# Performance work log

Measured on AMD Instinct MI355X. Metric: run time of the kernel, lower is better.

Reference implementation:

```python
import jax, jax.numpy as jnp
import numpy as np

B, S, D = 2, 2048, 1024
N_HEADS = 16
HEAD_DIM = D // N_HEADS


def setup_inputs() -> dict:
    key = jax.random.key(0)
    k1, k2, k3, k4, k5 = jax.random.split(key, 5)
    query = jax.random.normal(k1, (B, S, D), dtype=jnp.float32)
    key_t = jax.random.normal(k2, (B, S, D), dtype=jnp.float32)
    value = jax.random.normal(k3, (B, S, D), dtype=jnp.float32)
    # nn.Linear(dim, 3*dim): weight [3D, D], bias [3D]
    lim = 1.0 / np.sqrt(D)
    W_qkv_w = jax.random.uniform(k4, (3 * D, D), dtype=jnp.float32, minval=-lim, maxval=lim)
    W_qkv_b = jax.random.uniform(k5, (3 * D,), dtype=jnp.float32, minval=-lim, maxval=lim)
    return {"query": query, "key": key_t, "value": value, "W_qkv_w": W_qkv_w, "W_qkv_b": W_qkv_b}


def reference(query, key, value, W_qkv_w, W_qkv_b):
    # key/value args are ignored by the original module: Q, K, V all come
    # from the fused projection of `query` (faithful to source).
    b, s, d = query.shape
    qkv = query @ W_qkv_w.T + W_qkv_b                      # [B, S, 3D]
    qkv = qkv.reshape(b, s, 3, N_HEADS, HEAD_DIM)
    qkv = jnp.transpose(qkv, (2, 0, 3, 1, 4))              # [3, B, H, S, dh]
    q, k, v = qkv[0], qkv[1], qkv[2]
    # Faithful (inverted) scaling: scores DIVIDED by sqrt(1/d_model)
    scale_factor = jnp.sqrt(jnp.asarray(1.0 / (HEAD_DIM * N_HEADS), dtype=query.dtype))
    scores = jnp.einsum('bhqd,bhkd->bhqk', q, k) / scale_factor
    attn = jax.nn.softmax(scores, axis=-1)                 # dropout p=0.0 -> identity
    out = jnp.einsum('bhqk,bhkd->bhqd', attn, v)           # [B, H, S, dh]
    out = jnp.transpose(out, (0, 2, 1, 3)).reshape(b, s, d)
    return out
```

## Files before the change

### kernel.cpp

```cpp
#include <hip/hip_runtime.h>

#define B_  2
#define S_  2048
#define D_  1024
#define H_  16
#define DH_ 64
#define BH_ (B_*H_)

using f32x4   = __attribute__((ext_vector_type(4))) float;
using short4v = __attribute__((ext_vector_type(4))) short;
using short8v = __attribute__((ext_vector_type(8))) short;

__device__ float g_q [(size_t)BH_*S_*DH_];
__device__ float g_k [(size_t)BH_*S_*DH_];
__device__ float g_vt[(size_t)BH_*DH_*S_];

__device__ __forceinline__ short f2bf(float x){
  unsigned u = __builtin_bit_cast(unsigned, x);
  u += 0x7fffu + ((u >> 16) & 1u);
  return (short)(unsigned short)(u >> 16);
}
__device__ __forceinline__ float bf2f(short h){
  return __builtin_bit_cast(float, ((unsigned)(unsigned short)h) << 16);
}
__device__ __forceinline__ void split4f(const float4 v, short4v& h4, short4v& l4){
  float f[4] = {v.x, v.y, v.z, v.w};
#pragma unroll
  for (int i = 0; i < 4; ++i){
    short hh = f2bf(f[i]);
    h4[i] = hh;
    l4[i] = f2bf(f[i] - bf2f(hh));
  }
}

#define MFMA16(A,B,C) __builtin_amdgcn_mfma_f32_16x16x32_bf16((A),(B),(C),0,0,0)

__global__ __launch_bounds__(256) void qkv_proj_mfma(
    const float* __restrict__ X, const float* __restrict__ W,
    const float* __restrict__ bias)
{
  __shared__ short AH[128][40], AL[128][40], BHs[128][40], BLs[128][40];

  const int tid = threadIdx.x;
  const int w  = tid >> 6;
  const int ln = tid & 15;
  const int g  = (tid & 63) >> 4;
  const int wr = w >> 1, wc = w & 1;
  const int m0 = blockIdx.y * 128;
  const int n0 = blockIdx.x * 128;

  f32x4 zero4 = {0.f, 0.f, 0.f, 0.f};
  f32x4 acc[4][4];
#pragma unroll
  for (int mf = 0; mf < 4; ++mf)
#pragma unroll
    for (int nf = 0; nf < 4; ++nf) acc[mf][nf] = zero4;

  for (int k0 = 0; k0 < D_; k0 += 32) {
#pragma unroll
    for (int rep = 0; rep < 4; ++rep) {
      int idx = rep * 256 + tid;
      int r  = idx >> 3;
      int c4 = (idx & 7) << 2;
      float4 a = *(const float4*)&X[(size_t)(m0 + r) * D_ + k0 + c4];
      float4 b = *(const float4*)&W[(size_t)(n0 + r) * D_ + k0 + c4];
      short4v ah4, al4, bh4, bl4;
      split4f(a, ah4, al4);
      split4f(b, bh4, bl4);
      *(short4v*)&AH [r][c4] = ah4;
      *(short4v*)&AL [r][c4] = al4;
      *(short4v*)&BHs[r][c4] = bh4;
      *(short4v*)&BLs[r][c4] = bl4;
    }
    __syncthreads();

    short8v ah[4], al[4], bhf[4], blf[4];
#pragma unroll
    for (int mf = 0; mf < 4; ++mf) {
      ah[mf] = *(const short8v*)&AH[64*wr + 16*mf + ln][8*g];
      al[mf] = *(const short8v*)&AL[64*wr + 16*mf + ln][8*g];
    }
#pragma unroll
    for (int nf = 0; nf < 4; ++nf) {
      bhf[nf] = *(const short8v*)&BHs[64*wc + 16*nf + ln][8*g];
      blf[nf] = *(const short8v*)&BLs[64*wc + 16*nf + ln][8*g];
    }
#pragma unroll
    for (int mf = 0; mf < 4; ++mf)
#pragma unroll
      for (int nf = 0; nf < 4; ++nf) {
        acc[mf][nf] = MFMA16(ah[mf], bhf[nf], acc[mf][nf]);
        acc[mf][nf] = MFMA16(al[mf], bhf[nf], acc[mf][nf]);
        acc[mf][nf] = MFMA16(ah[mf], blf[nf], acc[mf][nf]);
      }
    __syncthreads();
  }

  const int which = n0 >> 10;
#pragma unroll
  for (int nf = 0; nf < 4; ++nf) {
    int col = n0 + 64*wc + 16*nf + ln;
    float bb = bias[col];
    int hh = (col & 1023) >> 6;
    int dh = col & 63;
#pragma unroll
    for (int mf = 0; mf < 4; ++mf) {
      int row0 = m0 + 64*wr + 16*mf + 4*g;
      int bidx = row0 >> 11;
      int s0   = row0 & 2047;
      if (which == 2) {
        f32x4 v;
#pragma unroll
        for (int i = 0; i < 4; ++i) v[i] = acc[mf][nf][i] + bb;
        *(f32x4*)&g_vt[(((size_t)bidx * H_ + hh) * DH_ + dh) * S_ + s0] = v;
      } else {
        float* dst = (which == 0) ? g_q : g_k;
        float sc   = (which == 0) ? 32.0f : 1.0f;
#pragma unroll
        for (int i = 0; i < 4; ++i)
          dst[(((size_t)bidx * H_ + hh) * S_ + s0 + i) * DH_ + dh] =
              (acc[mf][nf][i] + bb) * sc;
      }
    }
  }
}

__global__ __launch_bounds__(256) void attn_mfma(float* __restrict__ out)
{
  __shared__ short KH[64][72], KL[64][72], VT[64][72];
  __shared__ short PS[4][16][72];

  const int tid = threadIdx.x;
  const int w  = tid >> 6;
  const int ln = tid & 15;
  const int g  = (tid & 63) >> 4;
  const int bh = blockIdx.y;
  const int q0 = blockIdx.x * 64;
  const int b  = bh >> 4, h = bh & 15;

  const float* Qp = g_q  + (size_t)bh * S_ * DH_;
  const float* Kp = g_k  + (size_t)bh * S_ * DH_;
  const float* Vp = g_vt + (size_t)bh * DH_ * S_;

  short8v qh[2], ql[2];
  {
    const float* qr = &Qp[(size_t)(q0 + 16*w + ln) * DH_];
#pragma unroll
    for (int ks = 0; ks < 2; ++ks) {
      int d0 = 32*ks + 8*g;
      float4 f0 = *(const float4*)&qr[d0];
      float4 f1 = *(const float4*)&qr[d0 + 4];
      float f[8] = {f0.x,f0.y,f0.z,f0.w,f1.x,f1.y,f1.z,f1.w};
#pragma unroll
      for (int j = 0; j < 8; ++j) {
        short hh = f2bf(f[j]);
        qh[ks][j] = hh;
        ql[ks][j] = f2bf(f[j] - bf2f(hh));
      }
    }
  }

  f32x4 zero4 = {0.f,0.f,0.f,0.f};
  f32x4 o[4];
  float m_[4], l_[4];
#pragma unroll
  for (int i = 0; i < 4; ++i) { o[i] = zero4; m_[i] = -1e30f; l_[i] = 0.f; }

  for (int t0 = 0; t0 < S_; t0 += 64) {
#pragma unroll
    for (int rep = 0; rep < 4; ++rep) {
      int idx = rep * 256 + tid;
      int r  = idx >> 4;
      int c4 = (idx & 15) << 2;
      float4 kv = *(const float4*)&Kp[(size_t)(t0 + r) * DH_ + c4];
      short4v h4, l4;
      split4f(kv, h4, l4);
      *(short4v*)&KH[r][c4] = h4;
      *(short4v*)&KL[r][c4] = l4;
      float4 vv = *(const float4*)&Vp[(size_t)r * S_ + t0 + c4];
      short4v v4;
      v4[0] = f2bf(vv.x); v4[1] = f2bf(vv.y); v4[2] = f2bf(vv.z); v4[3] = f2bf(vv.w);
      *(short4v*)&VT[r][c4] = v4;
    }
    __syncthreads();

    f32x4 s[4];
#pragma unroll
    for (int nf = 0; nf < 4; ++nf) s[nf] = zero4;
#pragma unroll
    for (int ks = 0; ks < 2; ++ks) {
#pragma unroll
      for (int nf = 0; nf < 4; ++nf) {
        const short8v kh = *(const short8v*)&KH[16*nf + ln][32*ks + 8*g];
        const short8v kl = *(const short8v*)&KL[16*nf + ln][32*ks + 8*g];
        s[nf] = MFMA16(qh[ks], kh, s[nf]);
        s[nf] = MFMA16(ql[ks], kh, s[nf]);
        s[nf] = MFMA16(qh[ks], kl, s[nf]);
      }
    }

#pragma unroll
    for (int i = 0; i < 4; ++i) {
      float mt = fmaxf(fmaxf(s[0][i], s[1][i]), fmaxf(s[2][i], s[3][i]));
      mt = fmaxf(mt, __shfl_xor(mt, 1));
      mt = fmaxf(mt, __shfl_xor(mt, 2));
      mt = fmaxf(mt, __shfl_xor(mt, 4));
      mt = fmaxf(mt, __shfl_xor(mt, 8));
      float mn = fmaxf(m_[i], mt);
      float corr = __expf(m_[i] - mn);
      float sum = 0.f;
#pragma unroll
      for (int nf = 0; nf < 4; ++nf) {
        float p = __expf(s[nf][i] - mn);
        sum += p;
        s[nf][i] = p;
      }
      sum += __shfl_xor(sum, 1);
      sum += __shfl_xor(sum, 2);
      sum += __shfl_xor(sum, 4);
      sum += __shfl_xor(sum, 8);
      l_[i] = l_[i] * corr + sum;
      m_[i] = mn;
#pragma unroll
      for (int nf = 0; nf < 4; ++nf) {
        o[nf][i] *= corr;
        PS[w][4*g + i][16*nf + ln] = f2bf(s[nf][i]);
      }
    }

#pragma unroll
    for (int ks = 0; ks < 2; ++ks) {
      const short8v pa = *(const short8v*)&PS[w][ln][32*ks + 8*g];
#pragma unroll
      for (int nf = 0; nf < 4; ++nf) {
        const short8v vb = *(const short8v*)&VT[16*nf + ln][32*ks + 8*g];
        o[nf] = MFMA16(pa, vb, o[nf]);
      }
    }
    __syncthreads();
  }

#pragma unroll
  for (int i = 0; i < 4; ++i) {
    float inv = 1.0f / l_[i];
    int row = q0 + 16*w + 4*g + i;
    float* op = &out[((size_t)b * S_ + row) * D_ + h * DH_];
#pragma unroll
    for (int nf = 0; nf < 4; ++nf)
      op[16*nf + ln] = o[nf][i] * inv;
  }
}

extern "C" void kernel_launch(void* const* d_in, const int* in_sizes, int n_in,
                              void* d_out, int out_size, void* d_ws, size_t ws_size,
                              hipStream_t stream) {
    (void)d_ws; (void)ws_size; (void)n_in; (void)in_sizes;
    const float* X    = (const float*)d_in[0];
    const float* W    = (const float*)d_in[3];
    const float* bias = (const float*)d_in[4];
    float* out = (float*)d_out;

    dim3 gProj(24, 32);
    qkv_proj_mfma<<<gProj, 256, 0, stream>>>(X, W, bias);

    dim3 gAttn(S_ / 64, BH_);
    attn_mfma<<<gAttn, 256, 0, stream>>>(out);
}
```

Before: 306.0 us.

## Store pre-split bf16 Q/K/V, drop LDS staging, enlarge attention query tiles

Result: slower. 347.3 us (+13.5%).

```diff
diff --git a/kernel.cpp b/kernel.cpp
--- a/kernel.cpp
+++ b/kernel.cpp
@@ -6,14 +6,17 @@
 #define H_  16
 #define DH_ 64
 #define BH_ (B_*H_)
+#define NT_ (S_/64)
 
 using f32x4   = __attribute__((ext_vector_type(4))) float;
 using short4v = __attribute__((ext_vector_type(4))) short;
 using short8v = __attribute__((ext_vector_type(8))) short;
 
-__device__ float g_q [(size_t)BH_*S_*DH_];
-__device__ float g_k [(size_t)BH_*S_*DH_];
-__device__ float g_vt[(size_t)BH_*DH_*S_];
+__device__ short g_qh[(size_t)BH_*S_*DH_];
+__device__ short g_ql[(size_t)BH_*S_*DH_];
+__device__ short g_kh[(size_t)BH_*S_*DH_];
+__device__ short g_kl[(size_t)BH_*S_*DH_];
+__device__ short g_vt[(size_t)BH_*DH_*S_];
 
 __device__ __forceinline__ short f2bf(float x){
   unsigned u = __builtin_bit_cast(unsigned, x);
@@ -48,6 +51,7 @@
   const int wr = w >> 1, wc = w & 1;
   const int m0 = blockIdx.y * 128;
   const int n0 = blockIdx.x * 128;
+  const int which = n0 >> 10;
 
   f32x4 zero4 = {0.f, 0.f, 0.f, 0.f};
   f32x4 acc[4][4];
@@ -68,9 +72,11 @@
       split4f(a, ah4, al4);
       split4f(b, bh4, bl4);
       *(short4v*)&AH [r][c4] = ah4;
-      *(short4v*)&AL [r][c4] = al4;
       *(short4v*)&BHs[r][c4] = bh4;
-      *(short4v*)&BLs[r][c4] = bl4;
+      if (which < 2) {
+        *(short4v*)&AL [r][c4] = al4;
+        *(short4v*)&BLs[r][c4] = bl4;
+      }
     }
     __syncthreads();
 
@@ -78,25 +84,26 @@
 #pragma unroll
     for (int mf = 0; mf < 4; ++mf) {
       ah[mf] = *(const short8v*)&AH[64*wr + 16*mf + ln][8*g];
-      al[mf] = *(const short8v*)&AL[64*wr + 16*mf + ln][8*g];
+      if (which < 2) al[mf] = *(const short8v*)&AL[64*wr + 16*mf + ln][8*g];
     }
 #pragma unroll
     for (int nf = 0; nf < 4; ++nf) {
       bhf[nf] = *(const short8v*)&BHs[64*wc + 16*nf + ln][8*g];
-      blf[nf] = *(const short8v*)&BLs[64*wc + 16*nf + ln][8*g];
+      if (which < 2) blf[nf] = *(const short8v*)&BLs[64*wc + 16*nf + ln][8*g];
     }
 #pragma unroll
     for (int mf = 0; mf < 4; ++mf)
 #pragma unroll
       for (int nf = 0; nf < 4; ++nf) {
         acc[mf][nf] = MFMA16(ah[mf], bhf[nf], acc[mf][nf]);
-        acc[mf][nf] = MFMA16(al[mf], bhf[nf], acc[mf][nf]);
-        acc[mf][nf] = MFMA16(ah[mf], blf[nf], acc[mf][nf]);
+        if (which < 2) {
+          acc[mf][nf] = MFMA16(al[mf], bhf[nf], acc[mf][nf]);
+          acc[mf][nf] = MFMA16(ah[mf], blf[nf], acc[mf][nf]);
+        }
       }
     __syncthreads();
   }
 
-  const int which = n0 >> 10;
 #pragma unroll
   for (int nf = 0; nf < 4; ++nf) {
     int col = n0 + 64*wc + 16*nf + ln;
@@ -108,147 +115,171 @@
       int row0 = m0 + 64*wr + 16*mf + 4*g;
       int bidx = row0 >> 11;
       int s0   = row0 & 2047;
+      int bh   = bidx * H_ + hh;
       if (which == 2) {
-        f32x4 v;
-#pragma unroll
-        for (int i = 0; i < 4; ++i) v[i] = acc[mf][nf][i] + bb;
-        *(f32x4*)&g_vt[(((size_t)bidx * H_ + hh) * DH_ + dh) * S_ + s0] = v;
+        short4v v4;
+#pragma unroll
+        for (int i = 0; i < 4; ++i) v4[i] = f2bf(acc[mf][nf][i] + bb);
+        *(short4v*)&g_vt[((size_t)bh * DH_ + dh) * S_ + s0] = v4;
       } else {
-        float* dst = (which == 0) ? g_q : g_k;
-        float sc   = (which == 0) ? 32.0f : 1.0f;
-#pragma unroll
-        for (int i = 0; i < 4; ++i)
-          dst[(((size_t)bidx * H_ + hh) * S_ + s0 + i) * DH_ + dh] =
-              (acc[mf][nf][i] + bb) * sc;
-      }
-    }
-  }
-}
-
-__global__ __launch_bounds__(256) void attn_mfma(float* __restrict__ out)
+        short* dH = (which == 0) ? g_qh : g_kh;
+        short* dL = (which == 0) ? g_ql : g_kl;
+        float sc  = (which == 0) ? 32.0f : 1.0f;
+#pragma unroll
+        for (int i = 0; i < 4; ++i) {
+          float v = (acc[mf][nf][i] + bb) * sc;
+          short hi = f2bf(v);
+          short lo = f2bf(v - bf2f(hi));
+          size_t o = ((size_t)bh * S_ + s0 + i) * DH_ + dh;
+          dH[o] = hi;
+          dL[o] = lo;
+        }
+      }
+    }
+  }
+}
+
+__global__ __launch_bounds__(256, 2) void attn_mfma(float* __restrict__ out)
 {
-  __shared__ short KH[64][72], KL[64][72], VT[64][72];
-  __shared__ short PS[4][16][72];
+  __shared__ short PS[4][32][64];
 
   const int tid = threadIdx.x;
   const int w  = tid >> 6;
   const int ln = tid & 15;
   const int g  = (tid & 63) >> 4;
-  const int bh = blockIdx.y;
-  const int q0 = blockIdx.x * 64;
-  const int b  = bh >> 4, h = bh & 15;
-
-  const float* Qp = g_q  + (size_t)bh * S_ * DH_;
-  const float* Kp = g_k  + (size_t)bh * S_ * DH_;
-  const float* Vp = g_vt + (size_t)bh * DH_ * S_;
-
-  short8v qh[2], ql[2];
-  {
-    const float* qr = &Qp[(size_t)(q0 + 16*w + ln) * DH_];
+
+  const int bid = blockIdx.x;
+  const int swz = (bid & 7) * 64 + (bid >> 3);
+  const int bh  = swz >> 4;
+  const int q0  = (swz & 15) * 128;
+  const int b   = bh >> 4, h = bh & 15;
+
+  const size_t qb = (size_t)bh * S_ * DH_;
+  const short* __restrict__ Kh = g_kh + qb;
+  const short* __restrict__ Kl = g_kl + qb;
+  const short* __restrict__ Vt = g_vt + (size_t)bh * DH_ * S_;
+
+  short8v qh[2][2], ql[2][2];
+#pragma unroll
+  for (int rf = 0; rf < 2; ++rf)
 #pragma unroll
     for (int ks = 0; ks < 2; ++ks) {
-      int d0 = 32*ks + 8*g;
-      float4 f0 = *(const float4*)&qr[d0];
-      float4 f1 = *(const float4*)&qr[d0 + 4];
-      float f[8] = {f0.x,f0.y,f0.z,f0.w,f1.x,f1.y,f1.z,f1.w};
-#pragma unroll
-      for (int j = 0; j < 8; ++j) {
-        short hh = f2bf(f[j]);
-        qh[ks][j] = hh;
-        ql[ks][j] = f2bf(f[j] - bf2f(hh));
-      }
-    }
-  }
+      size_t o = qb + (size_t)(q0 + 32*w + 16*rf + ln) * DH_ + 32*ks + 8*g;
+      qh[rf][ks] = *(const short8v*)&g_qh[o];
+      ql[rf][ks] = *(const short8v*)&g_ql[o];
+    }
 
   f32x4 zero4 = {0.f,0.f,0.f,0.f};
-  f32x4 o[4];
-  float m_[4], l_[4];
-#pragma unroll
-  for (int i = 0; i < 4; ++i) { o[i] = zero4; m_[i] = -1e30f; l_[i] = 0.f; }
-
-  for (int t0 = 0; t0 < S_; t0 += 64) {
-#pragma unroll
-    for (int rep = 0; rep < 4; ++rep) {
-      int idx = rep * 256 + tid;
-      int r  = idx >> 4;
-      int c4 = (idx & 15) << 2;
-      float4 kv = *(const float4*)&Kp[(size_t)(t0 + r) * DH_ + c4];
-      short4v h4, l4;
-      split4f(kv, h4, l4);
-      *(short4v*)&KH[r][c4] = h4;
-      *(short4v*)&KL[r][c4] = l4;
-      float4 vv = *(const float4*)&Vp[(size_t)r * S_ + t0 + c4];
-      short4v v4;
-      v4[0] = f2bf(vv.x); v4[1] = f2bf(vv.y); v4[2] = f2bf(vv.z); v4[3] = f2bf(vv.w);
-      *(short4v*)&VT[r][c4] = v4;
-    }
-    __syncthreads();
-
-    f32x4 s[4];
-#pragma unroll
-    for (int nf = 0; nf < 4; ++nf) s[nf] = zero4;
-#pragma unroll
-    for (int ks = 0; ks < 2; ++ks) {
+  f32x4 o_[2][4];
+  float m_[2][4], l_[2][4];
+#pragma unroll
+  for (int rf = 0; rf < 2; ++rf)
+#pragma unroll
+    for (int i = 0; i < 4; ++i) {
+      o_[rf][i&3] = o_[rf][i&3];
+    }
+#pragma unroll
+  for (int rf = 0; rf < 2; ++rf)
+#pragma unroll
+    for (int nf = 0; nf < 4; ++nf) o_[rf][nf] = zero4;
+#pragma unroll
+  for (int rf = 0; rf < 2; ++rf)
+#pragma unroll
+    for (int i = 0; i < 4; ++i) { m_[rf][i] = -1e30f; l_[rf][i] = 0.f; }
+
+  for (int t = 0; t < NT_; ++t) {
+    const int t0 = t * 64;
+
+    short8v kh[2][4], kl[2][4];
+#pragma unroll
+    for (int ks = 0; ks < 2; ++ks)
 #pragma unroll
       for (int nf = 0; nf < 4; ++nf) {
-        const short8v kh = *(const short8v*)&KH[16*nf + ln][32*ks + 8*g];
-        const short8v kl = *(const short8v*)&KL[16*nf + ln][32*ks + 8*g];
-        s[nf] = MFMA16(qh[ks], kh, s[nf]);
-        s[nf] = MFMA16(ql[ks], kh, s[nf]);
-        s[nf] = MFMA16(qh[ks], kl, s[nf]);
-      }
-    }
-
+        size_t o = (size_t)(t0 + 16*nf + ln) * DH_ + 32*ks + 8*g;
+        kh[ks][nf] = *(const short8v*)&Kh[o];
+        kl[ks][nf] = *(const short8v*)&Kl[o];
+      }
+
+    f32x4 s[2][4];
+#pragma unroll
+    for (int rf = 0; rf < 2; ++rf)
+#pragma unroll
+      for (int nf = 0; nf < 4; ++nf) s[rf][nf] = zero4;
+#pragma unroll
+    for (int rf = 0; rf < 2; ++rf)
+#pragma unroll
+      for (int ks = 0; ks < 2; ++ks)
+#pragma unroll
+        for (int nf = 0; nf < 4; ++nf) {
+          s[rf][nf] = MFMA16(qh[rf][ks], kh[ks][nf], s[rf][nf]);
+          s[rf][nf] = MFMA16(ql[rf][ks], kh[ks][nf], s[rf][nf]);
+          s[rf][nf] = MFMA16(qh[rf][ks], kl[ks][nf], s[rf][nf]);
+        }
+
+    short8v vb[2][4];
+#pragma unroll
+    for (int ks = 0; ks < 2; ++ks)
+#pragma unroll
+      for (int nf = 0; nf < 4; ++nf)
+        vb[ks][nf] = *(const short8v*)&Vt[(size_t)(16*nf + ln) * S_ + t0 + 32*ks + 8*g];
+
+#pragma unroll
+    for (int rf = 0; rf < 2; ++rf)
+#pragma unroll
+      for (int i = 0; i < 4; ++i) {
+        float mt = fmaxf(fmaxf(s[rf][0][i], s[rf][1][i]),
+                         fmaxf(s[rf][2][i], s[rf][3][i]));
+        mt = fmaxf(mt, __shfl_xor(mt, 1));
+        mt = fmaxf(mt, __shfl_xor(mt, 2));
+        mt = fmaxf(mt, __shfl_xor(mt, 4));
+        mt = fmaxf(mt, __shfl_xor(mt, 8));
+        float mn = fmaxf(m_[rf][i], mt);
+        float corr = __expf(m_[rf][i] - mn);
+        float sum = 0.f;
+#pragma unroll
+        for (int nf = 0; nf < 4; ++nf) {
+          float p = __expf(s[rf][nf][i] - mn);
+          sum += p;
+          s[rf][nf][i] = p;
+        }
+        sum += __shfl_xor(sum, 1);
+        sum += __shfl_xor(sum, 2);
+        sum += __shfl_xor(sum, 4);
+        sum += __shfl_xor(sum, 8);
+        l_[rf][i] = l_[rf][i] * corr + sum;
+        m_[rf][i] = mn;
+        const int row = 16*rf + 4*g + i;
+        const int e   = (4*g + i) & 7;
+#pragma unroll
+        for (int nf = 0; nf < 4; ++nf) {
+          o_[rf][nf][i] *= corr;
+          PS[w][row][(16*nf + ln) ^ (e << 3)] = f2bf(s[rf][nf][i]);
+        }
+      }
+
+#pragma unroll
+    for (int rf = 0; rf < 2; ++rf)
+#pragma unroll
+      for (int ks = 0; ks < 2; ++ks) {
+        const short8v pa =
+            *(const short8v*)&PS[w][16*rf + ln][(32*ks + 8*g) ^ ((ln & 7) << 3)];
+#pragma unroll
+        for (int nf = 0; nf < 4; ++nf)
+          o_[rf][nf] = MFMA16(pa, vb[ks][nf], o_[rf][nf]);
+      }
+  }
+
+#pragma unroll
+  for (int rf = 0; rf < 2; ++rf)
 #pragma unroll
     for (int i = 0; i < 4; ++i) {
-      float mt = fmaxf(fmaxf(s[0][i], s[1][i]), fmaxf(s[2][i], s[3][i]));
-      mt = fmaxf(mt, __shfl_xor(mt, 1));
-      mt = fmaxf(mt, __shfl_xor(mt, 2));
-      mt = fmaxf(mt, __shfl_xor(mt, 4));
-      mt = fmaxf(mt, __shfl_xor(mt, 8));
-      float mn = fmaxf(m_[i], mt);
-      float corr = __expf(m_[i] - mn);
-      float sum = 0.f;
-#pragma unroll
-      for (int nf = 0; nf < 4; ++nf) {
-        float p = __expf(s[nf][i] - mn);
-        sum += p;
-        s[nf][i] = p;
-      }
-      sum += __shfl_xor(sum, 1);
-      sum += __shfl_xor(sum, 2);
-      sum += __shfl_xor(sum, 4);
-      sum += __shfl_xor(sum, 8);
-      l_[i] = l_[i] * corr + sum;
-      m_[i] = mn;
-#pragma unroll
-      for (int nf = 0; nf < 4; ++nf) {
-        o[nf][i] *= corr;
-        PS[w][4*g + i][16*nf + ln] = f2bf(s[nf][i]);
-      }
-    }
-
-#pragma unroll
-    for (int ks = 0; ks < 2; ++ks) {
-      const short8v pa = *(const short8v*)&PS[w][ln][32*ks + 8*g];
-#pragma unroll
-      for (int nf = 0; nf < 4; ++nf) {
-        const short8v vb = *(const short8v*)&VT[16*nf + ln][32*ks + 8*g];
-        o[nf] = MFMA16(pa, vb, o[nf]);
-      }
-    }
-    __syncthreads();
-  }
-
-#pragma unroll
-  for (int i = 0; i < 4; ++i) {
-    float inv = 1.0f / l_[i];
-    int row = q0 + 16*w + 4*g + i;
-    float* op = &out[((size_t)b * S_ + row) * D_ + h * DH_];
-#pragma unroll
-    for (int nf = 0; nf < 4; ++nf)
-      op[16*nf + ln] = o[nf][i] * inv;
-  }
+      float inv = 1.0f / l_[rf][i];
+      int row = q0 + 32*w + 16*rf + 4*g + i;
+      float* op = &out[((size_t)b * S_ + row) * D_ + h * DH_];
+#pragma unroll
+      for (int nf = 0; nf < 4; ++nf)
+        op[16*nf + ln] = o_[rf][nf][i] * inv;
+    }
 }
 
 extern "C" void kernel_launch(void* const* d_in, const int* in_sizes, int n_in,
@@ -263,6 +294,5 @@
     dim3 gProj(24, 32);
     qkv_proj_mfma<<<gProj, 256, 0, stream>>>(X, W, bias);
 
-    dim3 gAttn(S_ / 64, BH_);
-    attn_mfma<<<gAttn, 256, 0, stream>>>(out);
-}
+    attn_mfma<<<dim3(512), 256, 0, stream>>>(out);
+}
```
